# Kernel tuning notes

Measured on AMD Instinct MI355X. Metric: run time of the kernel, lower is better.

The kernel has to match this reference:

```python
import jax, jax.numpy as jnp
import numpy as np

N, E, B = 100000, 1600000, 512
NE, EE, H = 32, 32, 64
SCALE = float(2**48 - 1)


def _mlp2(x, W1, b1, W2, b2):
    # Linear -> ReLU -> Linear
    return jax.nn.relu(x @ W1 + b1) @ W2 + b2


def _gine(x, src, dst, e, W1, b1, W2, b2, n):
    # GINEConv (eps=0): nn(x + sum_j relu(x_j + e_ij))
    m = jax.nn.relu(x[src] + e)                      # [E, d] gather + edge add
    agg = jax.ops.segment_sum(m, dst, num_segments=n)  # scatter-add to targets
    return _mlp2(x + agg, W1, b1, W2, b2)


def _encode(names, edge_index, edge_attr, batch,
            idW1, idb1, idW2, idb2, edW1, edb1, edW2, edb2,
            c1W1, c1b1, c1W2, c1b2, c2W1, c2b1, c2W2, c2b2, linW, linb):
    norm = jnp.clip((names.astype(jnp.float32) + 2.0) / SCALE, 0.0, 1.0)[:, None]
    x = _mlp2(norm, idW1, idb1, idW2, idb2)          # [N, NE]
    e = _mlp2(edge_attr, edW1, edb1, edW2, edb2)     # [E, EE]
    src, dst = edge_index[0], edge_index[1]
    x = jax.nn.relu(_gine(x, src, dst, e, c1W1, c1b1, c1W2, c1b2, N))
    e2 = e @ linW + linb                             # edge lin for conv2 (EE->H)
    x = jax.nn.relu(_gine(x, src, dst, e2, c2W1, c2b1, c2W2, c2b2, N))
    sums = jax.ops.segment_sum(x, batch, num_segments=B)
    cnt = jax.ops.segment_sum(jnp.ones((x.shape[0],), x.dtype), batch, num_segments=B)
    return sums / jnp.maximum(cnt, 1.0)[:, None]     # global_mean_pool


def setup_inputs() -> dict:
    key = jax.random.key(0)
    ks = iter(jax.random.split(key, 64))
    def w(shape):
        return jax.random.normal(next(ks), shape, dtype=jnp.float32) * 0.05
    d = {}
    d['node_names_s'] = jax.random.randint(next(ks), (N,), 0, 1000000)
    d['edge_index_s'] = jax.random.randint(next(ks), (2, E), 0, N)
    d['edge_attr_s'] = jax.random.uniform(next(ks), (E, 1), dtype=jnp.float32)
    d['batch_s'] = jnp.sort(jax.random.randint(next(ks), (N,), 0, B))
    d['node_names_g'] = jax.random.randint(next(ks), (N,), 0, 1000000)
    d['edge_index_g'] = jax.random.randint(next(ks), (2, E), 0, N)
    d['edge_attr_g'] = jax.random.uniform(next(ks), (E, 1), dtype=jnp.float32)
    d['batch_g'] = jnp.sort(jax.random.randint(next(ks), (N,), 0, B))
    d['depth'] = jax.random.uniform(next(ks), (B,), dtype=jnp.float32)
    # shared encoders
    d['idW1'], d['idb1'], d['idW2'], d['idb2'] = w((1, NE)), w((NE,)), w((NE, NE)), w((NE,))
    d['edW1'], d['edb1'], d['edW2'], d['edb2'] = w((1, EE)), w((EE,)), w((EE, EE)), w((EE,))
    # state convs
    d['s1W1'], d['s1b1'], d['s1W2'], d['s1b2'] = w((NE, H)), w((H,)), w((H, H)), w((H,))
    d['s2W1'], d['s2b1'], d['s2W2'], d['s2b2'] = w((H, H)), w((H,)), w((H, H)), w((H,))
    d['s2linW'], d['s2linb'] = w((EE, H)), w((H,))
    # goal convs
    d['g1W1'], d['g1b1'], d['g1W2'], d['g1b2'] = w((NE, H)), w((H,)), w((H, H)), w((H,))
    d['g2W1'], d['g2b1'], d['g2W2'], d['g2b2'] = w((H, H)), w((H,)), w((H, H)), w((H,))
    d['g2linW'], d['g2linb'] = w((EE, H)), w((H,))
    d['rW1'], d['rb1'], d['rW2'], d['rb2'] = w((2 * H + 1, H)), w((H,)), w((H, 1)), w((1,))
    return d


def reference(node_names_s, edge_index_s, edge_attr_s, batch_s,
              node_names_g, edge_index_g, edge_attr_g, batch_g, depth,
              idW1, idb1, idW2, idb2, edW1, edb1, edW2, edb2,
              s1W1, s1b1, s1W2, s1b2, s2W1, s2b1, s2W2, s2b2, s2linW, s2linb,
              g1W1, g1b1, g1W2, g1b2, g2W1, g2b1, g2W2, g2b2, g2linW, g2linb,
              rW1, rb1, rW2, rb2):
    s = _encode(node_names_s, edge_index_s, edge_attr_s, batch_s,
                idW1, idb1, idW2, idb2, edW1, edb1, edW2, edb2,
                s1W1, s1b1, s1W2, s1b2, s2W1, s2b1, s2W2, s2b2, s2linW, s2linb)
    g = _encode(node_names_g, edge_index_g, edge_attr_g, batch_g,
                idW1, idb1, idW2, idb2, edW1, edb1, edW2, edb2,
                g1W1, g1b1, g1W2, g1b2, g2W1, g2b1, g2W2, g2b2, g2linW, g2linb)
    z = jnp.concatenate([s, g, depth[:, None]], axis=1)  # [B, 2H+1]
    return _mlp2(z, rW1, rb1, rW2, rb2)[:, 0]            # [B]
```

## Files before the change

### kernel.cpp

```cpp
#include <hip/hip_runtime.h>
#include <hip/hip_fp16.h>
#include <stdint.h>

namespace {

constexpr int NN   = 100000;
constexpr int TN   = 2 * NN;
constexpr int NEDG = 1600000;
constexpr int TE   = 2 * NEDG;
constexpr int NBAT = 512;
constexpr int NSEG = 33;

constexpr int NC     = 782;
constexpr int TILE   = 4096;
constexpr int ABLK   = (TE + TILE - 1) / TILE;
constexpr int ENTCAP = 5120;

constexpr int CONVBLK = 2048;

constexpr int S1H = 20;
constexpr int S2H = 36;

constexpr int TAB_BP = 0;
constexpr int TAB_D1 = 32;
constexpr int TAB_C1 = TAB_D1 + NSEG * 32;
constexpr int TAB_E2 = TAB_C1 + NSEG * 32;
constexpr int TAB_TOTAL = TAB_E2 + 4 * NSEG * 64;

__device__ __forceinline__ float relu_(float x) { return fmaxf(x, 0.0f); }

__device__ __forceinline__ float4 shfl_xor4(float4 v, int m) {
  return make_float4(__shfl_xor(v.x, m), __shfl_xor(v.y, m),
                     __shfl_xor(v.z, m), __shfl_xor(v.w, m));
}

__device__ __forceinline__ __half2 bch(int u) {
  return *reinterpret_cast<__half2*>(&u);
}
__device__ __forceinline__ int f2h2(float a, float b) {
  __half2 h = __floats2half2_rn(a, b);
  return *reinterpret_cast<int*>(&h);
}

__global__ void build_tables(const float* __restrict__ eW1, const float* __restrict__ eb1,
                             const float* __restrict__ eW2, const float* __restrict__ eb2,
                             const float* __restrict__ sLW, const float* __restrict__ sLb,
                             const float* __restrict__ gLW, const float* __restrict__ gLb,
                             float* __restrict__ tabs) {
  __shared__ float traw[32];
  __shared__ float ts[32];
  __shared__ float dt[NSEG * 32];
  __shared__ float ct[NSEG * 32];
  int tid = threadIdx.x;
  if (tid < 32) {
    float w = eW1[tid], b = eb1[tid];
    traw[tid] = (w != 0.0f) ? (-b / w) : 3.0e38f;
  }
  __syncthreads();
  if (tid < 32) {
    float v = traw[tid];
    int r = 0;
    for (int j = 0; j < 32; ++j) {
      float u = traw[j];
      r += (u < v) || (u == v && j < tid);
    }
    ts[r] = v;
  }
  __syncthreads();
  if (tid < 32) tabs[TAB_BP + tid] = ts[tid];
  for (int idx = tid; idx < NSEG * 32; idx += blockDim.x) {
    int s = idx >> 5, j = idx & 31;
    float a;
    if (s == 0)            a = ts[0] - 1.0f;
    else if (s == NSEG - 1) a = ts[31] + 1.0f;
    else                   a = 0.5f * ts[s - 1] + 0.5f * ts[s];
    float d = 0.0f, c = 0.0f;
    for (int i = 0; i < 32; ++i) {
      float w = eW1[i], b = eb1[i];
      if (fmaf(a, w, b) > 0.0f) {
        float w2 = eW2[i * 32 + j];
        d = fmaf(w, w2, d);
        c = fmaf(b, w2, c);
      }
    }
    c += eb2[j];
    dt[idx] = d; ct[idx] = c;
    tabs[TAB_D1 + idx] = d;
    tabs[TAB_C1 + idx] = c;
  }
  __syncthreads();
  for (int idx = tid; idx < NSEG * 64; idx += blockDim.x) {
    int s = idx >> 6, k = idx & 63;
    float ds = 0.f, cs = 0.f, dg = 0.f, cg = 0.f;
    for (int j = 0; j < 32; ++j) {
      float dv = dt[s * 32 + j], cv = ct[s * 32 + j];
      float ws = sLW[j * 64 + k], wg = gLW[j * 64 + k];
      ds = fmaf(dv, ws, ds); cs = fmaf(cv, ws, cs);
      dg = fmaf(dv, wg, dg); cg = fmaf(cv, wg, cg);
    }
    cs += sLb[k]; cg += gLb[k];
    tabs[TAB_E2 + idx]                 = ds;
    tabs[TAB_E2 + NSEG * 64 + idx]     = cs;
    tabs[TAB_E2 + 2 * NSEG * 64 + idx] = dg;
    tabs[TAB_E2 + 3 * NSEG * 64 + idx] = cg;
  }
}

__global__ __launch_bounds__(256) void fused_front(
    const int* __restrict__ names_s, const int* __restrict__ names_g,
    const float* __restrict__ idW1, const float* __restrict__ idb1,
    const float* __restrict__ idW2, const float* __restrict__ idb2,
    const int* __restrict__ src_s, const int* __restrict__ dst_s, const float* __restrict__ attr_s,
    const int* __restrict__ src_g, const int* __restrict__ dst_g, const float* __restrict__ attr_g,
    const int* __restrict__ bat_s, const int* __restrict__ bat_g,
    const float* __restrict__ tabs,
    __half* __restrict__ x0h,
    int* __restrict__ gcur, int2* __restrict__ part,
    int* __restrict__ start_s, int* __restrict__ start_g) {
  __shared__ int hist[NC];
  __shared__ int lofs[NC];
  __shared__ int lcur[NC];
  __shared__ int2 sorted[TILE];
  __shared__ int addr[TILE];
  __shared__ int scanbuf[256];
  __shared__ float bp[32];
  int t = threadIdx.x;
  if (blockIdx.x < ABLK) {
    if (t < 32) bp[t] = tabs[TAB_BP + t];
    for (int i = t; i < NC; i += 256) hist[i] = 0;
    __syncthreads();
    int base = blockIdx.x * TILE;
#pragma unroll
    for (int j = 0; j < 16; ++j) {
      int i = base + j * 256 + t;
      if (i < TE) {
        int d = (i < NEDG) ? dst_s[i] : (dst_g[i - NEDG] + NN);
        atomicAdd(&hist[d >> 8], 1);
      }
    }
    __syncthreads();
    int loc[4];
    int sum = 0;
#pragma unroll
    for (int j = 0; j < 4; ++j) {
      int b = t * 4 + j;
      int v = (b < NC) ? hist[b] : 0;
      loc[j] = sum; sum += v;
    }
    scanbuf[t] = sum;
    __syncthreads();
    for (int st = 1; st < 256; st <<= 1) {
      int u = (t >= st) ? scanbuf[t - st] : 0;
      __syncthreads();
      scanbuf[t] += u;
      __syncthreads();
    }
    int texcl = scanbuf[t] - sum;
#pragma unroll
    for (int j = 0; j < 4; ++j) {
      int b = t * 4 + j;
      if (b < NC) { lofs[b] = texcl + loc[j]; lcur[b] = 0; }
    }
    __syncthreads();
    for (int b = t; b < NC; b += 256) {
      int c = hist[b];
      hist[b] = c ? atomicAdd(&gcur[b], c) : 0;
    }
    __syncthreads();
#pragma unroll
    for (int j = 0; j < 16; ++j) {
      int i = base + j * 256 + t;
      if (i < TE) {
        int sl, d; float a;
        if (i < NEDG) { sl = src_s[i]; d = dst_s[i]; a = attr_s[i]; }
        else { int k = i - NEDG; sl = src_g[k]; d = dst_g[k] + NN; a = attr_g[k]; }
        int seg = 0;
#pragma unroll
        for (int q = 0; q < 32; ++q) seg += (bp[q] < a);
        int c = d >> 8;
        int r = atomicAdd(&lcur[c], 1);
        int s = lofs[c] + r;
        sorted[s] = make_int2(sl | ((d & 255) << 17) | (seg << 25), __float_as_int(a));
        addr[s] = c * ENTCAP + hist[c] + r;
      }
    }
    __syncthreads();
    int tot = (base + TILE <= TE) ? TILE : (TE - base);
    for (int s = t; s < tot; s += 256) part[addr[s]] = sorted[s];
  } else if (blockIdx.x < ABLK + 782) {
    int n = (blockIdx.x - ABLK) * 256 + t;
    if (n >= TN) return;
    int name = (n < NN) ? names_s[n] : names_g[n - NN];
    float norm = ((float)name + 2.0f) / 281474976710655.0f;
    norm = fminf(fmaxf(norm, 0.0f), 1.0f);
    float h[32];
#pragma unroll
    for (int i = 0; i < 32; ++i) h[i] = relu_(fmaf(norm, idW1[i], idb1[i]));
    int2* outh = (int2*)(x0h + (size_t)n * 32);
    for (int j0 = 0; j0 < 32; j0 += 4) {
      float a0 = idb2[j0], a1 = idb2[j0 + 1], a2 = idb2[j0 + 2], a3 = idb2[j0 + 3];
#pragma unroll
      for (int i = 0; i < 32; ++i) {
        float hv = h[i];
        a0 = fmaf(hv, idW2[i * 32 + j0],     a0);
        a1 = fmaf(hv, idW2[i * 32 + j0 + 1], a1);
        a2 = fmaf(hv, idW2[i * 32 + j0 + 2], a2);
        a3 = fmaf(hv, idW2[i * 32 + j0 + 3], a3);
      }
      outh[j0 >> 2] = make_int2(f2h2(a0, a1), f2h2(a2, a3));
    }
  } else {
    int blk = blockIdx.x - ABLK - 782;
    int half = blk >= 391;
    const int* bat = half ? bat_g : bat_s;
    int* start = half ? start_g : start_s;
    int i = (blk - half * 391) * 256 + t;
    if (i >= NN) return;
    int cur = bat[i];
    int prev = (i == 0) ? -1 : bat[i - 1];
    for (int b = prev + 1; b <= cur; ++b) start[b] = i;
    if (i == NN - 1) {
      for (int b = cur + 1; b <= NBAT; ++b) start[b] = NN;
    }
  }
}

__global__ __launch_bounds__(256) void partition_to_csr(
    const int* __restrict__ gcur,
    const int2* __restrict__ part,
    int* __restrict__ rowptr, int2* __restrict__ colattr) {
  __shared__ int2 outE[ENTCAP];
  __shared__ int hist[256];
  __shared__ int cur[256];
  __shared__ int sc[256];
  int t = threadIdx.x, b = blockIdx.x;
  {
    int acc = 0;
    for (int i = t; i < b; i += 256) acc += min(gcur[i], ENTCAP);
    sc[t] = acc;
    __syncthreads();
    for (int st = 128; st > 0; st >>= 1) {
      if (t < st) sc[t] += sc[t + st];
      __syncthreads();
    }
  }
  int obase = sc[0];
  if (b == 0 && t == 0) rowptr[TN] = TE;
  __syncthreads();
  hist[t] = 0;
  __syncthreads();
  int cnt = min(gcur[b], ENTCAP);
  int ibase = b * ENTCAP;
  for (int i = t; i < cnt; i += 256)
    atomicAdd(&hist[(part[ibase + i].x >> 17) & 255], 1);
  __syncthreads();
  int v = hist[t];
  sc[t] = v;
  __syncthreads();
  for (int st = 1; st < 256; st <<= 1) {
    int u = (t >= st) ? sc[t - st] : 0;
    __syncthreads();
    sc[t] += u;
    __syncthreads();
  }
  int excl = sc[t] - v;
  int gnode = b * 256 + t;
  if (gnode < TN) rowptr[gnode] = obase + excl;
  cur[t] = excl;
  __syncthreads();
  for (int i = t; i < cnt; i += 256) {
    int2 e = part[ibase + i];
    int dl = (e.x >> 17) & 255;
    int srcn = e.x & 0x1FFFF;
    int seg = (e.x >> 25) & 63;
    int pos = atomicAdd(&cur[dl], 1);
    float af = __int_as_float(e.y);
    outE[pos] = make_int2(srcn | (seg << 20), f2h2(af, af));
  }
  __syncthreads();
  for (int i = t; i < cnt; i += 256) colattr[obase + i] = outE[i];
}

__global__ __launch_bounds__(256) void conv1_dual(
    const __half* __restrict__ x0h,
    const int* __restrict__ rowptr, const int2* __restrict__ colattr,
    const float* __restrict__ tabs, float* __restrict__ hb) {
  __shared__ __half2 dt2[NSEG * S1H];
  __shared__ __half2 ct2[NSEG * S1H];
  for (int i = threadIdx.x; i < NSEG * 16; i += 256) {
    int s = i >> 4, j = i & 15;
    dt2[s * S1H + j] = __floats2half2_rn(tabs[TAB_D1 + s * 32 + 2 * j],
                                         tabs[TAB_D1 + s * 32 + 2 * j + 1]);
    ct2[s * S1H + j] = __floats2half2_rn(tabs[TAB_C1 + s * 32 + 2 * j],
                                         tabs[TAB_C1 + s * 32 + 2 * j + 1]);
  }
  __syncthreads();
  int lane = threadIdx.x & 63;
  int sub = lane & 7;
  int f0  = (lane >> 3) * 4;
  int h0  = (lane >> 3) * 2;
  int wid = blockIdx.x * 4 + (threadIdx.x >> 6);
  int nb = rowptr[wid], ne = rowptr[wid + 1];
  for (int n = wid; n < TN; n += 4 * CONVBLK) {
    int beg = nb, end = ne;
    int n2 = n + 4 * CONVBLK;
    if (n2 < TN) { nb = rowptr[n2]; ne = rowptr[n2 + 1]; }
    const __half* xb = x0h + (n >= NN ? (size_t)NN * 32 : 0);
    int2 sv = make_int2(0, 0);
    if (sub == 0) sv = *(const int2*)(x0h + (size_t)n * 32 + f0);
    float4 acc = make_float4(0.f, 0.f, 0.f, 0.f);
    for (int k = beg + sub; k < end; k += 16) {
      int2 ca0 = colattr[k];
      int kb = k + 8;
      bool has1 = kb < end;
      int2 ca1 = has1 ? colattr[kb] : ca0;
      unsigned p0 = (unsigned)ca0.x, p1 = (unsigned)ca1.x;
      int s0 = (int)(p0 & 0xFFFFFu), g0 = (int)(p0 >> 20);
      int s1 = (int)(p1 & 0xFFFFFu), g1 = (int)(p1 >> 20);
      __half2 az0 = bch(ca0.y);
      __half2 az1 = bch(ca1.y);
      int2 xv0 = *(const int2*)(xb + (size_t)s0 * 32 + f0);
      int2 xv1 = *(const int2*)(xb + (size_t)s1 * 32 + f0);
      int2 dv0 = *(const int2*)&dt2[g0 * S1H + h0];
      int2 cv0 = *(const int2*)&ct2[g0 * S1H + h0];
      __half2 v;
      float2 f;
      v = __hadd2(bch(xv0.x), __hfma2(az0, bch(dv0.x), bch(cv0.x)));
      f = __half22float2(v); acc.x += relu_(f.x); acc.y += relu_(f.y);
      v = __hadd2(bch(xv0.y), __hfma2(az0, bch(dv0.y), bch(cv0.y)));
      f = __half22float2(v); acc.z += relu_(f.x); acc.w += relu_(f.y);
      if (has1) {
        int2 dv1 = *(const int2*)&dt2[g1 * S1H + h0];
        int2 cv1 = *(const int2*)&ct2[g1 * S1H + h0];
        v = __hadd2(bch(xv1.x), __hfma2(az1, bch(dv1.x), bch(cv1.x)));
        f = __half22float2(v); acc.x += relu_(f.x); acc.y += relu_(f.y);
        v = __hadd2(bch(xv1.y), __hfma2(az1, bch(dv1.y), bch(cv1.y)));
        f = __half22float2(v); acc.z += relu_(f.x); acc.w += relu_(f.y);
      }
    }
#pragma unroll
    for (int m = 1; m < 8; m <<= 1) {
      float4 o = shfl_xor4(acc, m);
      acc.x += o.x; acc.y += o.y; acc.z += o.z; acc.w += o.w;
    }
    if (sub == 0) {
      float2 t0 = __half22float2(bch(sv.x)), t1 = __half22float2(bch(sv.y));
      *(float4*)(hb + (size_t)n * 32 + f0) =
          make_float4(t0.x + acc.x, t0.y + acc.y, t1.x + acc.z, t1.y + acc.w);
    }
  }
}

__global__ __launch_bounds__(256) void conv2_dual(
    const __half* __restrict__ x1h,
    const int* __restrict__ rowptr, const int2* __restrict__ colattr,
    const float* __restrict__ tabs, float* __restrict__ hb) {
  __shared__ __half2 dt2[NSEG * S2H];
  __shared__ __half2 ct2[NSEG * S2H];
  int halfg = blockIdx.x >= (CONVBLK / 2);
  const float* d2 = tabs + TAB_E2 + (size_t)halfg * 2 * NSEG * 64;
  for (int i = threadIdx.x; i < NSEG * 32; i += 256) {
    int s = i >> 5, j = i & 31;
    dt2[s * S2H + j] = __floats2half2_rn(d2[s * 64 + 2 * j], d2[s * 64 + 2 * j + 1]);
    ct2[s * S2H + j] = __floats2half2_rn(d2[NSEG * 64 + s * 64 + 2 * j],
                                         d2[NSEG * 64 + s * 64 + 2 * j + 1]);
  }
  __syncthreads();
  const __half* xb = x1h + (size_t)halfg * NN * 64;
  int lane = threadIdx.x & 63;
  int sub = lane & 7;
  int f0  = (lane >> 3) * 8;
  int h0  = (lane >> 3) * 4;
  int wid = (blockIdx.x - halfg * (CONVBLK / 2)) * 4 + (threadIdx.x >> 6);
  int nlim = halfg * NN + NN;
  int n0 = halfg * NN + wid;
  int nb = rowptr[n0], ne = rowptr[n0 + 1];
  for (int n = n0; n < nlim; n += 2 * CONVBLK) {
    int beg = nb, end = ne;
    int n2 = n + 2 * CONVBLK;
    if (n2 < nlim) { nb = rowptr[n2]; ne = rowptr[n2 + 1]; }
    int4 sv0 = make_int4(0, 0, 0, 0);
    if (sub == 0) sv0 = *(const int4*)(x1h + (size_t)n * 64 + f0);
    float4 accA = make_float4(0.f, 0.f, 0.f, 0.f);
    float4 accB = make_float4(0.f, 0.f, 0.f, 0.f);
    for (int k = beg + sub; k < end; k += 16) {
      int2 ca0 = colattr[k];
      int kb = k + 8;
      bool has1 = kb < end;
      int2 ca1 = has1 ? colattr[kb] : ca0;
      unsigned p0 = (unsigned)ca0.x, p1 = (unsigned)ca1.x;
      int s0 = (int)(p0 & 0xFFFFFu), g0 = (int)(p0 >> 20);
      int s1 = (int)(p1 & 0xFFFFFu), g1 = (int)(p1 >> 20);
      __half2 az0 = bch(ca0.y);
      __half2 az1 = bch(ca1.y);
      int4 xv0 = *(const int4*)(xb + (size_t)s0 * 64 + f0);
      int4 xv1 = *(const int4*)(xb + (size_t)s1 * 64 + f0);
      int4 dv0 = *(const int4*)&dt2[g0 * S2H + h0];
      int4 cv0 = *(const int4*)&ct2[g0 * S2H + h0];
      __half2 v;
      float2 f;
      v = __hadd2(bch(xv0.x), __hfma2(az0, bch(dv0.x), bch(cv0.x)));
      f = __half22float2(v); accA.x += relu_(f.x); accA.y += relu_(f.y);
      v = __hadd2(bch(xv0.y), __hfma2(az0, bch(dv0.y), bch(cv0.y)));
      f = __half22float2(v); accA.z += relu_(f.x); accA.w += relu_(f.y);
      v = __hadd2(bch(xv0.z), __hfma2(az0, bch(dv0.z), bch(cv0.z)));
      f = __half22float2(v); accB.x += relu_(f.x); accB.y += relu_(f.y);
      v = __hadd2(bch(xv0.w), __hfma2(az0, bch(dv0.w), bch(cv0.w)));
      f = __half22float2(v); accB.z += relu_(f.x); accB.w += relu_(f.y);
      if (has1) {
        int4 dv1 = *(const int4*)&dt2[g1 * S2H + h0];
        int4 cv1 = *(const int4*)&ct2[g1 * S2H + h0];
        v = __hadd2(bch(xv1.x), __hfma2(az1, bch(dv1.x), bch(cv1.x)));
        f = __half22float2(v); accA.x += relu_(f.x); accA.y += relu_(f.y);
        v = __hadd2(bch(xv1.y), __hfma2(az1, bch(dv1.y), bch(cv1.y)));
        f = __half22float2(v); accA.z += relu_(f.x); accA.w += relu_(f.y);
        v = __hadd2(bch(xv1.z), __hfma2(az1, bch(dv1.z), bch(cv1.z)));
        f = __half22float2(v); accB.x += relu_(f.x); accB.y += relu_(f.y);
        v = __hadd2(bch(xv1.w), __hfma2(az1, bch(dv1.w), bch(cv1.w)));
        f = __half22float2(v); accB.z += relu_(f.x); accB.w += relu_(f.y);
      }
    }
#pragma unroll
    for (int m = 1; m < 8; m <<= 1) {
      float4 oA = shfl_xor4(accA, m);
      float4 oB = shfl_xor4(accB, m);
      accA.x += oA.x; accA.y += oA.y; accA.z += oA.z; accA.w += oA.w;
      accB.x += oB.x; accB.y += oB.y; accB.z += oB.z; accB.w += oB.w;
    }
    if (sub == 0) {
      float2 t0 = __half22float2(bch(sv0.x)), t1 = __half22float2(bch(sv0.y));
      float2 t2 = __half22float2(bch(sv0.z)), t3 = __half22float2(bch(sv0.w));
      float* op = hb + (size_t)n * 64 + f0;
      *(float4*)op       = make_float4(t0.x + accA.x, t0.y + accA.y, t1.x + accA.z, t1.y + accA.w);
      *(float4*)(op + 4) = make_float4(t2.x + accB.x, t2.y + accB.y, t3.x + accB.z, t3.y + accB.w);
    }
  }
}

__global__ __launch_bounds__(256) void mlp1_dual(
    const float* __restrict__ hin,
    const float* __restrict__ sW1, const float* __restrict__ sb1,
    const float* __restrict__ sW2, const float* __restrict__ sb2,
    const float* __restrict__ gW1, const float* __restrict__ gb1,
    const float* __restrict__ gW2, const float* __restrict__ gb2,
    __half* __restrict__ hout) {
  constexpr int IN = 32;
  __shared__ float hsT[IN][65];
  __shared__ float ysT[64][65];
  int base = blockIdx.x * 64;
  for (int idx = threadIdx.x; idx < 64 * IN; idx += 256) {
    int node = idx / IN, k = idx - node * IN;
    hsT[k][node] = hin[(size_t)(base + node) * IN + k];
  }
  __syncthreads();
  int nt = threadIdx.x >> 4, jx = threadIdx.x & 15;
  int n0 = nt * 4, f0 = jx * 4;
  bool isg = (base + n0) >= NN;
  const float* W1 = isg ? gW1 : sW1;
  const float* b1 = isg ? gb1 : sb1;
  const float* W2 = isg ? gW2 : sW2;
  const float* b2 = isg ? gb2 : sb2;
  float4 acc0, acc1, acc2, acc3;
  {
    const float4 b = *(const float4*)(b1 + f0);
    acc0 = b; acc1 = b; acc2 = b; acc3 = b;
  }
  for (int k = 0; k < IN; ++k) {
    const float4 h = *(const float4*)&hsT[k][n0];
    const float4 w = *(const float4*)(W1 + k * 64 + f0);
    acc0.x = fmaf(h.x, w.x, acc0.x); acc0.y = fmaf(h.x, w.y, acc0.y);
    acc0.z = fmaf(h.x, w.z, acc0.z); acc0.w = fmaf(h.x, w.w, acc0.w);
    acc1.x = fmaf(h.y, w.x, acc1.x); acc1.y = fmaf(h.y, w.y, acc1.y);
    acc1.z = fmaf(h.y, w.z, acc1.z); acc1.w = fmaf(h.y, w.w, acc1.w);
    acc2.x = fmaf(h.z, w.x, acc2.x); acc2.y = fmaf(h.z, w.y, acc2.y);
    acc2.z = fmaf(h.z, w.z, acc2.z); acc2.w = fmaf(h.z, w.w, acc2.w);
    acc3.x = fmaf(h.w, w.x, acc3.x); acc3.y = fmaf(h.w, w.y, acc3.y);
    acc3.z = fmaf(h.w, w.z, acc3.z); acc3.w = fmaf(h.w, w.w, acc3.w);
  }
  ysT[f0 + 0][n0 + 0] = relu_(acc0.x); ysT[f0 + 1][n0 + 0] = relu_(acc0.y);
  ysT[f0 + 2][n0 + 0] = relu_(acc0.z); ysT[f0 + 3][n0 + 0] = relu_(acc0.w);
  ysT[f0 + 0][n0 + 1] = relu_(acc1.x); ysT[f0 + 1][n0 + 1] = relu_(acc1.y);
  ysT[f0 + 2][n0 + 1] = relu_(acc1.z); ysT[f0 + 3][n0 + 1] = relu_(acc1.w);
  ysT[f0 + 0][n0 + 2] = relu_(acc2.x); ysT[f0 + 1][n0 + 2] = relu_(acc2.y);
  ysT[f0 + 2][n0 + 2] = relu_(acc2.z); ysT[f0 + 3][n0 + 2] = relu_(acc2.w);
  ysT[f0 + 0][n0 + 3] = relu_(acc3.x); ysT[f0 + 1][n0 + 3] = relu_(acc3.y);
  ysT[f0 + 2][n0 + 3] = relu_(acc3.z); ysT[f0 + 3][n0 + 3] = relu_(acc3.w);
  __syncthreads();
  {
    const float4 b = *(const float4*)(b2 + f0);
    acc0 = b; acc1 = b; acc2 = b; acc3 = b;
  }
  for (int k = 0; k < 64; ++k) {
    const float4 h = *(const float4*)&ysT[k][n0];
    const float4 w = *(const float4*)(W2 + k * 64 + f0);
    acc0.x = fmaf(h.x, w.x, acc0.x); acc0.y = fmaf(h.x, w.y, acc0.y);
    acc0.z = fmaf(h.x, w.z, acc0.z); acc0.w = fmaf(h.x, w.w, acc0.w);
    acc1.x = fmaf(h.y, w.x, acc1.x); acc1.y = fmaf(h.y, w.y, acc1.y);
    acc1.z = fmaf(h.y, w.z, acc1.z); acc1.w = fmaf(h.y, w.w, acc1.w);
    acc2.x = fmaf(h.z, w.x, acc2.x); acc2.y = fmaf(h.z, w.y, acc2.y);
    acc2.z = fmaf(h.z, w.z, acc2.z); acc2.w = fmaf(h.z, w.w, acc2.w);
    acc3.x = fmaf(h.w, w.x, acc3.x); acc3.y = fmaf(h.w, w.y, acc3.y);
    acc3.z = fmaf(h.w, w.z, acc3.z); acc3.w = fmaf(h.w, w.w, acc3.w);
  }
  float4 o;
  o = make_float4(relu_(acc0.x), relu_(acc0.y), relu_(acc0.z), relu_(acc0.w));
  *(int2*)(hout + (size_t)(base + n0 + 0) * 64 + f0) = make_int2(f2h2(o.x, o.y), f2h2(o.z, o.w));
  o = make_float4(relu_(acc1.x), relu_(acc1.y), relu_(acc1.z), relu_(acc1.w));
  *(int2*)(hout + (size_t)(base + n0 + 1) * 64 + f0) = make_int2(f2h2(o.x, o.y), f2h2(o.z, o.w));
  o = make_float4(relu_(acc2.x), relu_(acc2.y), relu_(acc2.z), relu_(acc2.w));
  *(int2*)(hout + (size_t)(base + n0 + 2) * 64 + f0) = make_int2(f2h2(o.x, o.y), f2h2(o.z, o.w));
  o = make_float4(relu_(acc3.x), relu_(acc3.y), relu_(acc3.z), relu_(acc3.w));
  *(int2*)(hout + (size_t)(base + n0 + 3) * 64 + f0) = make_int2(f2h2(o.x, o.y), f2h2(o.z, o.w));
}

__global__ __launch_bounds__(256) void mlp2_pool_dual(
    const float* __restrict__ hin,
    const float* __restrict__ sW1, const float* __restrict__ sb1,
    const float* __restrict__ sW2, const float* __restrict__ sb2,
    const float* __restrict__ gW1, const float* __restrict__ gb1,
    const float* __restrict__ gW2, const float* __restrict__ gb2,
    const int* __restrict__ bat_s, const int* __restrict__ bat_g,
    float* __restrict__ psum) {
  constexpr int IN = 64;
  __shared__ float hsT[IN][65];
  __shared__ float ysT[64][65];
  __shared__ int pid[64];
  int base = blockIdx.x * 64;
  for (int idx = threadIdx.x; idx < 64 * IN; idx += 256) {
    int node = idx / IN, k = idx - node * IN;
    hsT[k][node] = hin[(size_t)(base + node) * IN + k];
  }
  if (threadIdx.x < 64) {
    int gb = base + threadIdx.x;
    pid[threadIdx.x] = (gb < NN) ? bat_s[gb] : (NBAT + bat_g[gb - NN]);
  }
  __syncthreads();
  int nt = threadIdx.x >> 4, jx = threadIdx.x & 15;
  int n0 = nt * 4, f0 = jx * 4;
  bool isg = (base + n0) >= NN;
  const float* W1 = isg ? gW1 : sW1;
  const float* b1 = isg ? gb1 : sb1;
  const float* W2 = isg ? gW2 : sW2;
  const float* b2 = isg ? gb2 : sb2;
  float4 acc0, acc1, acc2, acc3;
  {
    const float4 b = *(const float4*)(b1 + f0);
    acc0 = b; acc1 = b; acc2 = b; acc3 = b;
  }
  for (int k = 0; k < IN; ++k) {
    const float4 h = *(const float4*)&hsT[k][n0];
    const float4 w = *(const float4*)(W1 + k * 64 + f0);
    acc0.x = fmaf(h.x, w.x, acc0.x); acc0.y = fmaf(h.x, w.y, acc0.y);
    acc0.z = fmaf(h.x, w.z, acc0.z); acc0.w = fmaf(h.x, w.w, acc0.w);
    acc1.x = fmaf(h.y, w.x, acc1.x); acc1.y = fmaf(h.y, w.y, acc1.y);
    acc1.z = fmaf(h.y, w.z, acc1.z); acc1.w = fmaf(h.y, w.w, acc1.w);
    acc2.x = fmaf(h.z, w.x, acc2.x); acc2.y = fmaf(h.z, w.y, acc2.y);
    acc2.z = fmaf(h.z, w.z, acc2.z); acc2.w = fmaf(h.z, w.w, acc2.w);
    acc3.x = fmaf(h.w, w.x, acc3.x); acc3.y = fmaf(h.w, w.y, acc3.y);
    acc3.z = fmaf(h.w, w.z, acc3.z); acc3.w = fmaf(h.w, w.w, acc3.w);
  }
  ysT[f0 + 0][n0 + 0] = relu_(acc0.x); ysT[f0 + 1][n0 + 0] = relu_(acc0.y);
  ysT[f0 + 2][n0 + 0] = relu_(acc0.z); ysT[f0 + 3][n0 + 0] = relu_(acc0.w);
  ysT[f0 + 0][n0 + 1] = relu_(acc1.x); ysT[f0 + 1][n0 + 1] = relu_(acc1.y);
  ysT[f0 + 2][n0 + 1] = relu_(acc1.z); ysT[f0 + 3][n0 + 1] = relu_(acc1.w);
  ysT[f0 + 0][n0 + 2] = relu_(acc2.x); ysT[f0 + 1][n0 + 2] = relu_(acc2.y);
  ysT[f0 + 2][n0 + 2] = relu_(acc2.z); ysT[f0 + 3][n0 + 2] = relu_(acc2.w);
  ysT[f0 + 0][n0 + 3] = relu_(acc3.x); ysT[f0 + 1][n0 + 3] = relu_(acc3.y);
  ysT[f0 + 2][n0 + 3] = relu_(acc3.z); ysT[f0 + 3][n0 + 3] = relu_(acc3.w);
  __syncthreads();
  {
    const float4 b = *(const float4*)(b2 + f0);
    acc0 = b; acc1 = b; acc2 = b; acc3 = b;
  }
  for (int k = 0; k < 64; ++k) {
    const float4 h = *(const float4*)&ysT[k][n0];
    const float4 w = *(const float4*)(W2 + k * 64 + f0);
    acc0.x = fmaf(h.x, w.x, acc0.x); acc0.y = fmaf(h.x, w.y, acc0.y);
    acc0.z = fmaf(h.x, w.z, acc0.z); acc0.w = fmaf(h.x, w.w, acc0.w);
    acc1.x = fmaf(h.y, w.x, acc1.x); acc1.y = fmaf(h.y, w.y, acc1.y);
    acc1.z = fmaf(h.y, w.z, acc1.z); acc1.w = fmaf(h.y, w.w, acc1.w);
    acc2.x = fmaf(h.z, w.x, acc2.x); acc2.y = fmaf(h.z, w.y, acc2.y);
    acc2.z = fmaf(h.z, w.z, acc2.z); acc2.w = fmaf(h.z, w.w, acc2.w);
    acc3.x = fmaf(h.w, w.x, acc3.x); acc3.y = fmaf(h.w, w.y, acc3.y);
    acc3.z = fmaf(h.w, w.z, acc3.z); acc3.w = fmaf(h.w, w.w, acc3.w);
  }
  __syncthreads();
  ysT[f0 + 0][n0 + 0] = relu_(acc0.x); ysT[f0 + 1][n0 + 0] = relu_(acc0.y);
  ysT[f0 + 2][n0 + 0] = relu_(acc0.z); ysT[f0 + 3][n0 + 0] = relu_(acc0.w);
  ysT[f0 + 0][n0 + 1] = relu_(acc1.x); ysT[f0 + 1][n0 + 1] = relu_(acc1.y);
  ysT[f0 + 2][n0 + 1] = relu_(acc1.z); ysT[f0 + 3][n0 + 1] = relu_(acc1.w);
  ysT[f0 + 0][n0 + 2] = relu_(acc2.x); ysT[f0 + 1][n0 + 2] = relu_(acc2.y);
  ysT[f0 + 2][n0 + 2] = relu_(acc2.z); ysT[f0 + 3][n0 + 2] = relu_(acc2.w);
  ysT[f0 + 0][n0 + 3] = relu_(acc3.x); ysT[f0 + 1][n0 + 3] = relu_(acc3.y);
  ysT[f0 + 2][n0 + 3] = relu_(acc3.z); ysT[f0 + 3][n0 + 3] = relu_(acc3.w);
  __syncthreads();
  int c = threadIdx.x >> 6, f = threadIdx.x & 63;
  int cur = pid[c * 16];
  float run = 0.0f;
  for (int i = 0; i < 16; ++i) {
    int nx = c * 16 + i;
    int p = pid[nx];
    if (p != cur) { atomicAdd(&psum[(size_t)cur * 64 + f], run); run = 0.0f; cur = p; }
    run += ysT[f][nx];
  }
  atomicAdd(&psum[(size_t)cur * 64 + f], run);
}

__global__ __launch_bounds__(256) void regressor16(
    const float* __restrict__ psum,
    const int* __restrict__ start_s, const int* __restrict__ start_g,
    const float* __restrict__ depth,
    const float* __restrict__ W1, const float* __restrict__ b1,
    const float* __restrict__ W2, const float* __restrict__ b2,
    float* __restrict__ out) {
  __shared__ float zs[16][132];
  __shared__ float ys[64][17];
  __shared__ float inv_s[16], inv_g[16];
  int base = blockIdx.x * 16;
  if (threadIdx.x < 16) {
    int b = base + threadIdx.x;
    inv_s[threadIdx.x] = 1.0f / fmaxf((float)(start_s[b + 1] - start_s[b]), 1.0f);
    inv_g[threadIdx.x] = 1.0f / fmaxf((float)(start_g[b + 1] - start_g[b]), 1.0f);
  }
  __syncthreads();
  for (int i = threadIdx.x; i < 16 * 64; i += 256) {
    int ln = i >> 6, k = i & 63;
    zs[ln][k]      = psum[(size_t)(base + ln) * 64 + k] * inv_s[ln];
    zs[ln][64 + k] = psum[(size_t)(NBAT + base + ln) * 64 + k] * inv_g[ln];
  }
  if (threadIdx.x < 16) zs[threadIdx.x][128] = depth[base + threadIdx.x];
  __syncthreads();
  int g = threadIdx.x >> 4;
  int j = threadIdx.x & 15;
  int f0 = j * 4;
  float a0, a1, a2, a3;
  {
    const float4 b = *(const float4*)(b1 + f0);
    a0 = b.x; a1 = b.y; a2 = b.z; a3 = b.w;
  }
  for (int k = 0; k < 129; ++k) {
    float zv = zs[g][k];
    const float4 w = *(const float4*)(W1 + k * 64 + f0);
    a0 = fmaf(zv, w.x, a0); a1 = fmaf(zv, w.y, a1);
    a2 = fmaf(zv, w.z, a2); a3 = fmaf(zv, w.w, a3);
  }
  ys[f0 + 0][g] = relu_(a0);
  ys[f0 + 1][g] = relu_(a1);
  ys[f0 + 2][g] = relu_(a2);
  ys[f0 + 3][g] = relu_(a3);
  __syncthreads();
  float s = ys[f0 + 0][g] * W2[f0 + 0] + ys[f0 + 1][g] * W2[f0 + 1] +
            ys[f0 + 2][g] * W2[f0 + 2] + ys[f0 + 3][g] * W2[f0 + 3];
#pragma unroll
  for (int m = 1; m < 16; m <<= 1) s += __shfl_xor(s, m);
  if (j == 0) out[base + g] = s + b2[0];
}

}

extern "C" void kernel_launch(void* const* d_in, const int* in_sizes, int n_in,
                              void* d_out, int out_size, void* d_ws, size_t ws_size,
                              hipStream_t stream) {
  const int*   names_s = (const int*)d_in[0];
  const int*   ei_s    = (const int*)d_in[1];
  const float* ea_s    = (const float*)d_in[2];
  const int*   bat_s   = (const int*)d_in[3];
  const int*   names_g = (const int*)d_in[4];
  const int*   ei_g    = (const int*)d_in[5];
  const float* ea_g    = (const float*)d_in[6];
  const int*   bat_g   = (const int*)d_in[7];
  const float* depth   = (const float*)d_in[8];
  const float* idW1 = (const float*)d_in[9],  *idb1 = (const float*)d_in[10];
  const float* idW2 = (const float*)d_in[11], *idb2 = (const float*)d_in[12];
  const float* edW1 = (const float*)d_in[13], *edb1 = (const float*)d_in[14];
  const float* edW2 = (const float*)d_in[15], *edb2 = (const float*)d_in[16];
  const float* s1W1 = (const float*)d_in[17], *s1b1 = (const float*)d_in[18];
  const float* s1W2 = (const float*)d_in[19], *s1b2 = (const float*)d_in[20];
  const float* s2W1 = (const float*)d_in[21], *s2b1 = (const float*)d_in[22];
  const float* s2W2 = (const float*)d_in[23], *s2b2 = (const float*)d_in[24];
  const float* s2LW = (const float*)d_in[25], *s2Lb = (const float*)d_in[26];
  const float* g1W1 = (const float*)d_in[27], *g1b1 = (const float*)d_in[28];
  const float* g1W2 = (const float*)d_in[29], *g1b2 = (const float*)d_in[30];
  const float* g2W1 = (const float*)d_in[31], *g2b1 = (const float*)d_in[32];
  const float* g2W2 = (const float*)d_in[33], *g2b2 = (const float*)d_in[34];
  const float* g2LW = (const float*)d_in[35], *g2Lb = (const float*)d_in[36];
  const float* rW1  = (const float*)d_in[37], *rb1  = (const float*)d_in[38];
  const float* rW2  = (const float*)d_in[39], *rb2  = (const float*)d_in[40];
  (void)in_sizes; (void)n_in; (void)out_size; (void)ws_size;

  char* ws = (char*)d_ws;
  size_t off = 0;
  auto alloc = [&](size_t bytes) -> char* {
    char* p = ws + off;
    off += (bytes + 255) & ~(size_t)255;
    return p;
  };
  float* tabs    = (float*)alloc((size_t)TAB_TOTAL * 4);
  char*  act   = alloc((size_t)TN * 64 * 4 + (size_t)TN * 32 * 4);
  float* h2buf = (float*)act;
  float* h1buf = (float*)(act + (size_t)TN * 64 * 4);
  int2*  part  = (int2*)act;
  __half* x0h  = (__half*)alloc((size_t)TN * 32 * 2);
  __half* x1h  = (__half*)alloc((size_t)TN * 64 * 2);
  int2*  colattr = (int2*) alloc((size_t)TE * 8);
  int*   gcur    = (int*)  alloc((size_t)NC * 4);
  int*   rowptr  = (int*)  alloc((size_t)(TN + 1) * 4);
  int*   start_s = (int*)  alloc((size_t)(NBAT + 1) * 4);
  int*   start_g = (int*)  alloc((size_t)(NBAT + 1) * 4);
  float* psum    = (float*)alloc((size_t)2 * NBAT * 64 * 4);

  build_tables<<<1, 256, 0, stream>>>(edW1, edb1, edW2, edb2, s2LW, s2Lb, g2LW, g2Lb, tabs);
  hipMemsetAsync(gcur, 0, (size_t)NC * 4, stream);
  hipMemsetAsync(psum, 0, (size_t)2 * NBAT * 64 * 4, stream);

  fused_front<<<ABLK + 782 + 782, 256, 0, stream>>>(
      names_s, names_g, idW1, idb1, idW2, idb2,
      ei_s, ei_s + NEDG, ea_s, ei_g, ei_g + NEDG, ea_g,
      bat_s, bat_g, tabs, x0h, gcur, part, start_s, start_g);
  partition_to_csr<<<NC, 256, 0, stream>>>(gcur, part, rowptr, colattr);

  conv1_dual<<<CONVBLK, 256, 0, stream>>>(x0h, rowptr, colattr, tabs, h1buf);
  mlp1_dual<<<TN / 64, 256, 0, stream>>>(h1buf,
                                         s1W1, s1b1, s1W2, s1b2,
                                         g1W1, g1b1, g1W2, g1b2, x1h);
  conv2_dual<<<CONVBLK, 256, 0, stream>>>(x1h, rowptr, colattr, tabs, h2buf);
  mlp2_pool_dual<<<TN / 64, 256, 0, stream>>>(h2buf,
                                              s2W1, s2b1, s2W2, s2b2,
                                              g2W1, g2b1, g2W2, g2b2,
                                              bat_s, bat_g, psum);
  regressor16<<<32, 256, 0, stream>>>(psum, start_s, start_g, depth,
                                      rW1, rb1, rW2, rb2, (float*)d_out);
}
```

Baseline: 569.5 us.

## Replace two-pass CSR partition with direct ELL scatter via per-node atomics

```diff
diff --git a/kernel.cpp b/kernel.cpp
--- a/kernel.cpp
+++ b/kernel.cpp
@@ -11,10 +11,8 @@
 constexpr int NBAT = 512;
 constexpr int NSEG = 33;
 
-constexpr int NC     = 782;
-constexpr int TILE   = 4096;
-constexpr int ABLK   = (TE + TILE - 1) / TILE;
-constexpr int ENTCAP = 5120;
+constexpr int ELLW = 48;
+constexpr int SBLK = 1024;
 
 constexpr int CONVBLK = 2048;
 
@@ -115,80 +113,33 @@
     const int* __restrict__ bat_s, const int* __restrict__ bat_g,
     const float* __restrict__ tabs,
     __half* __restrict__ x0h,
-    int* __restrict__ gcur, int2* __restrict__ part,
+    int* __restrict__ cnt, int2* __restrict__ ell,
     int* __restrict__ start_s, int* __restrict__ start_g) {
-  __shared__ int hist[NC];
-  __shared__ int lofs[NC];
-  __shared__ int lcur[NC];
-  __shared__ int2 sorted[TILE];
-  __shared__ int addr[TILE];
-  __shared__ int scanbuf[256];
   __shared__ float bp[32];
   int t = threadIdx.x;
-  if (blockIdx.x < ABLK) {
+  if (blockIdx.x < SBLK) {
     if (t < 32) bp[t] = tabs[TAB_BP + t];
-    for (int i = t; i < NC; i += 256) hist[i] = 0;
     __syncthreads();
-    int base = blockIdx.x * TILE;
+    constexpr int STRD = SBLK * 256;
+    for (int i0 = blockIdx.x * 256 + t; i0 < TE; i0 += 4 * STRD) {
 #pragma unroll
-    for (int j = 0; j < 16; ++j) {
-      int i = base + j * 256 + t;
-      if (i < TE) {
-        int d = (i < NEDG) ? dst_s[i] : (dst_g[i - NEDG] + NN);
-        atomicAdd(&hist[d >> 8], 1);
+      for (int u = 0; u < 4; ++u) {
+        int i = i0 + u * STRD;
+        if (i < TE) {
+          int sl, d; float a;
+          if (i < NEDG) { sl = src_s[i]; d = dst_s[i]; a = attr_s[i]; }
+          else { int k = i - NEDG; sl = src_g[k]; d = dst_g[k] + NN; a = attr_g[k]; }
+          int seg = 0;
+#pragma unroll
+          for (int q = 0; q < 32; ++q) seg += (bp[q] < a);
+          int pos = atomicAdd(&cnt[d], 1);
+          if (pos < ELLW)
+            ell[(size_t)d * ELLW + pos] = make_int2(sl | (seg << 20), f2h2(a, a));
+        }
       }
     }
-    __syncthreads();
-    int loc[4];
-    int sum = 0;
-#pragma unroll
-    for (int j = 0; j < 4; ++j) {
-      int b = t * 4 + j;
-      int v = (b < NC) ? hist[b] : 0;
-      loc[j] = sum; sum += v;
-    }
-    scanbuf[t] = sum;
-    __syncthreads();
-    for (int st = 1; st < 256; st <<= 1) {
-      int u = (t >= st) ? scanbuf[t - st] : 0;
-      __syncthreads();
-      scanbuf[t] += u;
-      __syncthreads();
-    }
-    int texcl = scanbuf[t] - sum;
-#pragma unroll
-    for (int j = 0; j < 4; ++j) {
-      int b = t * 4 + j;
-      if (b < NC) { lofs[b] = texcl + loc[j]; lcur[b] = 0; }
-    }
-    __syncthreads();
-    for (int b = t; b < NC; b += 256) {
-      int c = hist[b];
-      hist[b] = c ? atomicAdd(&gcur[b], c) : 0;
-    }
-    __syncthreads();
-#pragma unroll
-    for (int j = 0; j < 16; ++j) {
-      int i = base + j * 256 + t;
-      if (i < TE) {
-        int sl, d; float a;
-        if (i < NEDG) { sl = src_s[i]; d = dst_s[i]; a = attr_s[i]; }
-        else { int k = i - NEDG; sl = src_g[k]; d = dst_g[k] + NN; a = attr_g[k]; }
-        int seg = 0;
-#pragma unroll
-        for (int q = 0; q < 32; ++q) seg += (bp[q] < a);
-        int c = d >> 8;
-        int r = atomicAdd(&lcur[c], 1);
-        int s = lofs[c] + r;
-        sorted[s] = make_int2(sl | ((d & 255) << 17) | (seg << 25), __float_as_int(a));
-        addr[s] = c * ENTCAP + hist[c] + r;
-      }
-    }
-    __syncthreads();
-    int tot = (base + TILE <= TE) ? TILE : (TE - base);
-    for (int s = t; s < tot; s += 256) part[addr[s]] = sorted[s];
-  } else if (blockIdx.x < ABLK + 782) {
-    int n = (blockIdx.x - ABLK) * 256 + t;
+  } else if (blockIdx.x < SBLK + 782) {
+    int n = (blockIdx.x - SBLK) * 256 + t;
     if (n >= TN) return;
     int name = (n < NN) ? names_s[n] : names_g[n - NN];
     float norm = ((float)name + 2.0f) / 281474976710655.0f;
@@ -210,7 +161,7 @@
       outh[j0 >> 2] = make_int2(f2h2(a0, a1), f2h2(a2, a3));
     }
   } else {
-    int blk = blockIdx.x - ABLK - 782;
+    int blk = blockIdx.x - SBLK - 782;
     int half = blk >= 391;
     const int* bat = half ? bat_g : bat_s;
     int* start = half ? start_g : start_s;
@@ -225,65 +176,9 @@
   }
 }
 
-__global__ __launch_bounds__(256) void partition_to_csr(
-    const int* __restrict__ gcur,
-    const int2* __restrict__ part,
-    int* __restrict__ rowptr, int2* __restrict__ colattr) {
-  __shared__ int2 outE[ENTCAP];
-  __shared__ int hist[256];
-  __shared__ int cur[256];
-  __shared__ int sc[256];
-  int t = threadIdx.x, b = blockIdx.x;
-  {
-    int acc = 0;
-    for (int i = t; i < b; i += 256) acc += min(gcur[i], ENTCAP);
-    sc[t] = acc;
-    __syncthreads();
-    for (int st = 128; st > 0; st >>= 1) {
-      if (t < st) sc[t] += sc[t + st];
-      __syncthreads();
-    }
-  }
-  int obase = sc[0];
-  if (b == 0 && t == 0) rowptr[TN] = TE;
-  __syncthreads();
-  hist[t] = 0;
-  __syncthreads();
-  int cnt = min(gcur[b], ENTCAP);
-  int ibase = b * ENTCAP;
-  for (int i = t; i < cnt; i += 256)
-    atomicAdd(&hist[(part[ibase + i].x >> 17) & 255], 1);
-  __syncthreads();
-  int v = hist[t];
-  sc[t] = v;
-  __syncthreads();
-  for (int st = 1; st < 256; st <<= 1) {
-    int u = (t >= st) ? sc[t - st] : 0;
-    __syncthreads();
-    sc[t] += u;
-    __syncthreads();
-  }
-  int excl = sc[t] - v;
-  int gnode = b * 256 + t;
-  if (gnode < TN) rowptr[gnode] = obase + excl;
-  cur[t] = excl;
-  __syncthreads();
-  for (int i = t; i < cnt; i += 256) {
-    int2 e = part[ibase + i];
-    int dl = (e.x >> 17) & 255;
-    int srcn = e.x & 0x1FFFF;
-    int seg = (e.x >> 25) & 63;
-    int pos = atomicAdd(&cur[dl], 1);
-    float af = __int_as_float(e.y);
-    outE[pos] = make_int2(srcn | (seg << 20), f2h2(af, af));
-  }
-  __syncthreads();
-  for (int i = t; i < cnt; i += 256) colattr[obase + i] = outE[i];
-}
-
 __global__ __launch_bounds__(256) void conv1_dual(
     const __half* __restrict__ x0h,
-    const int* __restrict__ rowptr, const int2* __restrict__ colattr,
+    const int* __restrict__ cnt, const int2* __restrict__ ell,
     const float* __restrict__ tabs, float* __restrict__ hb) {
   __shared__ __half2 dt2[NSEG * S1H];
   __shared__ __half2 ct2[NSEG * S1H];
@@ -300,20 +195,21 @@
   int f0  = (lane >> 3) * 4;
   int h0  = (lane >> 3) * 2;
   int wid = blockIdx.x * 4 + (threadIdx.x >> 6);
-  int nb = rowptr[wid], ne = rowptr[wid + 1];
+  int cn = cnt[wid];
   for (int n = wid; n < TN; n += 4 * CONVBLK) {
-    int beg = nb, end = ne;
+    int deg = min(cn, ELLW);
     int n2 = n + 4 * CONVBLK;
-    if (n2 < TN) { nb = rowptr[n2]; ne = rowptr[n2 + 1]; }
+    if (n2 < TN) cn = cnt[n2];
+    int beg = n * ELLW, end = beg + deg;
     const __half* xb = x0h + (n >= NN ? (size_t)NN * 32 : 0);
     int2 sv = make_int2(0, 0);
     if (sub == 0) sv = *(const int2*)(x0h + (size_t)n * 32 + f0);
     float4 acc = make_float4(0.f, 0.f, 0.f, 0.f);
     for (int k = beg + sub; k < end; k += 16) {
-      int2 ca0 = colattr[k];
+      int2 ca0 = ell[k];
       int kb = k + 8;
       bool has1 = kb < end;
-      int2 ca1 = has1 ? colattr[kb] : ca0;
+      int2 ca1 = has1 ? ell[kb] : ca0;
       unsigned p0 = (unsigned)ca0.x, p1 = (unsigned)ca1.x;
       int s0 = (int)(p0 & 0xFFFFFu), g0 = (int)(p0 >> 20);
       int s1 = (int)(p1 & 0xFFFFFu), g1 = (int)(p1 >> 20);
@@ -353,7 +249,7 @@
 
 __global__ __launch_bounds__(256) void conv2_dual(
     const __half* __restrict__ x1h,
-    const int* __restrict__ rowptr, const int2* __restrict__ colattr,
+    const int* __restrict__ cnt, const int2* __restrict__ ell,
     const float* __restrict__ tabs, float* __restrict__ hb) {
   __shared__ __half2 dt2[NSEG * S2H];
   __shared__ __half2 ct2[NSEG * S2H];
@@ -374,20 +270,21 @@
   int wid = (blockIdx.x - halfg * (CONVBLK / 2)) * 4 + (threadIdx.x >> 6);
   int nlim = halfg * NN + NN;
   int n0 = halfg * NN + wid;
-  int nb = rowptr[n0], ne = rowptr[n0 + 1];
+  int cn = cnt[n0];
   for (int n = n0; n < nlim; n += 2 * CONVBLK) {
-    int beg = nb, end = ne;
+    int deg = min(cn, ELLW);
     int n2 = n + 2 * CONVBLK;
-    if (n2 < nlim) { nb = rowptr[n2]; ne = rowptr[n2 + 1]; }
+    if (n2 < nlim) cn = cnt[n2];
+    int beg = n * ELLW, end = beg + deg;
     int4 sv0 = make_int4(0, 0, 0, 0);
     if (sub == 0) sv0 = *(const int4*)(x1h + (size_t)n * 64 + f0);
     float4 accA = make_float4(0.f, 0.f, 0.f, 0.f);
     float4 accB = make_float4(0.f, 0.f, 0.f, 0.f);
     for (int k = beg + sub; k < end; k += 16) {
-      int2 ca0 = colattr[k];
+      int2 ca0 = ell[k];
       int kb = k + 8;
       bool has1 = kb < end;
-      int2 ca1 = has1 ? colattr[kb] : ca0;
+      int2 ca1 = has1 ? ell[kb] : ca0;
       unsigned p0 = (unsigned)ca0.x, p1 = (unsigned)ca1.x;
       int s0 = (int)(p0 & 0xFFFFFu), g0 = (int)(p0 >> 20);
       int s1 = (int)(p1 & 0xFFFFFu), g1 = (int)(p1 >> 20);
@@ -696,34 +593,31 @@
     return p;
   };
   float* tabs    = (float*)alloc((size_t)TAB_TOTAL * 4);
-  char*  act   = alloc((size_t)TN * 64 * 4 + (size_t)TN * 32 * 4);
-  float* h2buf = (float*)act;
-  float* h1buf = (float*)(act + (size_t)TN * 64 * 4);
-  int2*  part  = (int2*)act;
+  int2*  ell     = (int2*) alloc((size_t)TN * ELLW * 8);
+  float* hreg    = (float*)alloc((size_t)TN * 64 * 4);
+  float* h1buf   = hreg;
+  float* h2buf   = hreg;
   __half* x0h  = (__half*)alloc((size_t)TN * 32 * 2);
   __half* x1h  = (__half*)alloc((size_t)TN * 64 * 2);
-  int2*  colattr = (int2*) alloc((size_t)TE * 8);
-  int*   gcur    = (int*)  alloc((size_t)NC * 4);
-  int*   rowptr  = (int*)  alloc((size_t)(TN + 1) * 4);
+  int*   cnt     = (int*)  alloc((size_t)TN * 4);
   int*   start_s = (int*)  alloc((size_t)(NBAT + 1) * 4);
   int*   start_g = (int*)  alloc((size_t)(NBAT + 1) * 4);
   float* psum    = (float*)alloc((size_t)2 * NBAT * 64 * 4);
 
   build_tables<<<1, 256, 0, stream>>>(edW1, edb1, edW2, edb2, s2LW, s2Lb, g2LW, g2Lb, tabs);
-  hipMemsetAsync(gcur, 0, (size_t)NC * 4, stream);
+  hipMemsetAsync(cnt, 0, (size_t)TN * 4, stream);
   hipMemsetAsync(psum, 0, (size_t)2 * NBAT * 64 * 4, stream);
 
-  fused_front<<<ABLK + 782 + 782, 256, 0, stream>>>(
+  fused_front<<<SBLK + 782 + 782, 256, 0, stream>>>(
       names_s, names_g, idW1, idb1, idW2, idb2,
       ei_s, ei_s + NEDG, ea_s, ei_g, ei_g + NEDG, ea_g,
-      bat_s, bat_g, tabs, x0h, gcur, part, start_s, start_g);
-  partition_to_csr<<<NC, 256, 0, stream>>>(gcur, part, rowptr, colattr);
-
-  conv1_dual<<<CONVBLK, 256, 0, stream>>>(x0h, rowptr, colattr, tabs, h1buf);
+      bat_s, bat_g, tabs, x0h, cnt, ell, start_s, start_g);
+
+  conv1_dual<<<CONVBLK, 256, 0, stream>>>(x0h, cnt, ell, tabs, h1buf);
   mlp1_dual<<<TN / 64, 256, 0, stream>>>(h1buf,
                                          s1W1, s1b1, s1W2, s1b2,
                                          g1W1, g1b1, g1W2, g1b2, x1h);
-  conv2_dual<<<CONVBLK, 256, 0, stream>>>(x1h, rowptr, colattr, tabs, h2buf);
+  conv2_dual<<<CONVBLK, 256, 0, stream>>>(x1h, cnt, ell, tabs, h2buf);
   mlp2_pool_dual<<<TN / 64, 256, 0, stream>>>(h2buf,
                                               s2W1, s2b1, s2W2, s2b2,
                                               g2W1, g2b1, g2W2, g2b2,
```

Result: slower. 640.0 us (+12.4%).
